# Performance work log

Hardware: AMD Instinct MI355X
Metric: run time of the kernel (lower is better)

## Reference

```python
import jax, jax.numpy as jnp
import numpy as np
from jax import lax

MIN_R = 0.01
RADIUS = 0.8
NSAMPLE = 32
PRED_NSAMPLE = 16
TEMPERATURE = 1.0
DIV_COEF = 10.0
GRID3 = 64  # grid_size**3, grid_size=4
EPS = 1e-5


def _ball_query(q, xyz, radius, nsample):
    """q (M,3), xyz (N,3), radius scalar or (M,). Returns idx (M,nsample) int32, empty (M,) bool.
    Mirrors stack ball_query CUDA op: first-found neighbors within radius, padded with first index."""
    N = xyz.shape[0]
    d2 = jnp.sum((q[:, None, :] - xyz[None, :, :]) ** 2, axis=-1)  # (M,N)
    r = jnp.broadcast_to(jnp.asarray(radius, d2.dtype), (q.shape[0],))[:, None]
    valid = d2 < r * r
    score = jnp.where(valid, -jnp.arange(N, dtype=jnp.int32), -(N + 1))
    vals, _ = lax.top_k(score, nsample)  # largest score == smallest valid index
    idx = -vals
    pad = idx == (N + 1)
    idx = jnp.where(pad, idx[:, :1], idx)  # pad with first found neighbor
    empty = pad[:, 0]                       # no neighbor at all
    idx = jnp.where(empty[:, None], 0, idx)
    return idx, empty


def _group(q, xyz, feats, idx, empty):
    """QueryAndGroup gather: relative xyz concat point features; zero empty queries.
    Returns (M, nsample, 3+C)."""
    g_xyz = xyz[idx] - q[:, None, :]
    g = jnp.concatenate([g_xyz, feats[idx]], axis=-1)
    return jnp.where(empty[:, None, None], jnp.zeros((), g.dtype), g)


def _mlp(x, params):
    """Shared 1x1 Conv2d + BatchNorm2d(training stats) + ReLU stack. x: (B,M,S,C)."""
    for W, g, b in params:
        x = jnp.einsum('bmsc,cd->bmsd', x, W)
        mu = x.mean(axis=(0, 1, 2))
        var = x.var(axis=(0, 1, 2))
        x = (x - mu) * lax.rsqrt(var + EPS) * g + b
        x = jax.nn.relu(x)
    return x


def setup_inputs() -> dict:
    key = jax.random.key(0)
    ks = jax.random.split(key, 16)
    B, N, C, R, Croi = 2, 8192, 32, 64, 128
    scene = jnp.array([10.0, 10.0, 4.0], jnp.float32)
    xyz = jax.random.uniform(ks[0], (B, N, 3), jnp.float32) * scene
    features = jax.random.normal(ks[1], (B, N, C), jnp.float32)
    rois = jax.random.uniform(ks[2], (B, R, GRID3, 3), jnp.float32) * scene
    roi_features = jax.random.normal(ks[3], (B, R, Croi), jnp.float32)

    def kaiming(k, fi, fo):
        return jax.random.normal(k, (fi, fo), jnp.float32) * np.float32(np.sqrt(2.0 / fi))

    return {
        'xyz': xyz, 'features': features, 'rois': rois, 'roi_features': roi_features,
        'temperature_decay': jnp.ones((1,), jnp.float32),
        # predict mlp: [32+3, 32, 32]
        'pw0': kaiming(ks[4], 35, 32), 'pg0': jnp.ones(32), 'pb0': jnp.zeros(32),
        'pw1': kaiming(ks[5], 32, 32), 'pg1': jnp.ones(32), 'pb1': jnp.zeros(32),
        # feat mlp: [32+3, 64, 64]
        'fw0': kaiming(ks[6], 35, 64), 'fg0': jnp.ones(64), 'fb0': jnp.zeros(64),
        'fw1': kaiming(ks[7], 64, 64), 'fg1': jnp.ones(64), 'fb1': jnp.zeros(64),
        # predict fc: [32*64 + 128, 1]
        'fcw': kaiming(ks[8], 2176, 1), 'fcb': jnp.zeros(1),
    }


def reference(xyz, features, rois, roi_features, temperature_decay,
              pw0, pg0, pb0, pw1, pg1, pb1,
              fw0, fg0, fb0, fw1, fg1, fb1, fcw, fcb):
    B, num_rois = rois.shape[0], rois.shape[1]
    new_xyz = rois.reshape(B, -1, 3)  # (B, M, 3), M = num_rois*grid^3

    # ---- radius-prediction branch: fixed-radius grouping + MLP + max-pool ----
    idx_p, empty_p = jax.vmap(lambda q, x: _ball_query(q, x, RADIUS, PRED_NSAMPLE))(new_xyz, xyz)
    gp = jax.vmap(_group)(new_xyz, xyz, features, idx_p, empty_p)  # (B,M,S,3+C)
    gp = _mlp(gp, [(pw0, pg0, pb0), (pw1, pg1, pb1)])
    pooled = gp.max(axis=2)                       # (B, M, Cp)
    pooled = pooled.reshape(B, num_rois, -1)      # (B, R, grid^3*Cp)
    res = jnp.concatenate([pooled, roi_features], axis=-1) @ fcw + fcb  # (B,R,1)
    r = jnp.maximum(res / DIV_COEF + RADIUS, MIN_R)
    r_pts = jnp.broadcast_to(r, (B, num_rois, GRID3)).reshape(B, -1)    # (B, M)

    # ---- deformable branch: per-query radius grouping + soft weights ----
    idx_d, empty_d = jax.vmap(lambda q, x, rr: _ball_query(q, x, rr, NSAMPLE))(new_xyz, xyz, r_pts)
    gd = jax.vmap(_group)(new_xyz, xyz, features, idx_d, empty_d)       # (B,M,S,3+C)
    dist = jnp.linalg.norm(gd[..., :3], axis=-1)                        # (B,M,S)
    w = jax.nn.sigmoid((r_pts[..., None] - dist) / (TEMPERATURE * temperature_decay[0]))
    w = jnp.where(empty_d[..., None], jnp.zeros((), w.dtype), w)
    gd = _mlp(gd, [(fw0, fg0, fb0), (fw1, fg1, fb1)])                   # (B,M,S,Cout)
    new_feats = (w[..., None] * gd).max(axis=2)                          # (B,M,Cout)

    return new_xyz.reshape(-1, 3), new_feats.reshape(-1, new_feats.shape[-1])
```

## Files before the change

### kernel.cpp

```cpp
#include <hip/hip_runtime.h>
#include <hip/hip_fp16.h>

#define NB 2
#define NPTS 8192
#define NQ 4096
#define MTOT 8192
#define SP 16
#define SD 32
#define CIN 32
#define CP 32
#define CF 64
#define NROI 128
#define RADIUS_C 0.8f
#define MIN_R_C 0.01f
#define DIV_COEF_C 10.0f

#define INV_CS 1.25f
#define NCX 13
#define NCY 13
#define NCZ 5
#define NCELL (NCX * NCY * NCZ)

__device__ int    g_idx_p[MTOT * SP];
__device__ int    g_empty_p[MTOT];
__device__ int    g_idx_d[MTOT * SD];
__device__ int    g_empty_d[MTOT];
__device__ int    g_cellcnt[NB][NCELL];
__device__ int    g_cellcur[NB][NCELL];
__device__ int    g_cellstart[NB][NCELL + 1];
__device__ float4 g_cellxyzw[NB][NPTS];
__device__ unsigned char g_xa[(size_t)MTOT * SD * CF * 2];
__device__ unsigned char g_xb[(size_t)MTOT * SD * CF * 2];
__device__ unsigned int g_w1h[CF * CF / 2];
__device__ float  g_psT[CF * 2048];
__device__ float  g_pqT[CF * 2048];
__device__ float  g_bnscale[4][CF];
__device__ float  g_bnshift[4][CF];
__device__ float  g_rroi[NROI];

typedef _Float16 h2v __attribute__((ext_vector_type(2)));
__device__ __forceinline__ float fdot2f(unsigned int a, unsigned int b, float c) {
#if defined(__has_builtin)
#if __has_builtin(__builtin_amdgcn_fdot2)
    h2v ha, hb;
    ha = *(h2v*)&a; hb = *(h2v*)&b;
    return __builtin_amdgcn_fdot2(ha, hb, c, false);
#else
    __half2 ha = *(__half2*)&a, hb = *(__half2*)&b;
    float2 fa = __half22float2(ha), fb = __half22float2(hb);
    return fmaf(fa.x, fb.x, fmaf(fa.y, fb.y, c));
#endif
#else
    __half2 ha = *(__half2*)&a, hb = *(__half2*)&b;
    float2 fa = __half22float2(ha), fb = __half22float2(hb);
    return fmaf(fa.x, fb.x, fmaf(fa.y, fb.y, c));
#endif
}

__device__ __forceinline__ int cell_of(float x, float y, float z) {
    int cx = min(NCX - 1, max(0, (int)floorf(x * INV_CS)));
    int cy = min(NCY - 1, max(0, (int)floorf(y * INV_CS)));
    int cz = min(NCZ - 1, max(0, (int)floorf(z * INV_CS)));
    return (cz * NCY + cy) * NCX + cx;
}

#define SETUP_N (MTOT * 3 + CF * CF / 2 + NB * NCELL)
__global__ void setup_kernel(const float* __restrict__ rois, const float* __restrict__ fw1,
                             float* __restrict__ out) {
    int i = blockIdx.x * 256 + threadIdx.x;
    if (i < MTOT * 3) { out[i] = rois[i]; return; }
    i -= MTOT * 3;
    if (i < CF * CF / 2) {
        int ch = i >> 5, c2 = i & 31;
        __half2 h = __floats2half2_rn(fw1[(2 * c2) * CF + ch], fw1[(2 * c2 + 1) * CF + ch]);
        g_w1h[i] = *(unsigned int*)&h;
        return;
    }
    i -= CF * CF / 2;
    if (i < NB * NCELL) ((int*)g_cellcnt)[i] = 0;
}

__global__ void grid_count_kernel(const float* __restrict__ xyz) {
    int i = blockIdx.x * 256 + threadIdx.x;
    int b = i >> 13;
    int cell = cell_of(xyz[(size_t)i * 3 + 0], xyz[(size_t)i * 3 + 1], xyz[(size_t)i * 3 + 2]);
    atomicAdd(&g_cellcnt[b][cell], 1);
}

__global__ void grid_prefix_kernel() {
    __shared__ int sc[1024];
    int b = blockIdx.x, tid = threadIdx.x;
    int v = (tid < NCELL) ? g_cellcnt[b][tid] : 0;
    sc[tid] = v;
    __syncthreads();
    for (int off = 1; off < 1024; off <<= 1) {
        int add = (tid >= off) ? sc[tid - off] : 0;
        __syncthreads();
        sc[tid] += add;
        __syncthreads();
    }
    if (tid < NCELL) {
        int excl = sc[tid] - v;
        g_cellstart[b][tid] = excl;
        g_cellcur[b][tid] = excl;
    }
    if (tid == 0) g_cellstart[b][NCELL] = NPTS;
}

__global__ void grid_scatter_kernel(const float* __restrict__ xyz) {
    int i = blockIdx.x * 256 + threadIdx.x;
    int b = i >> 13, il = i & (NPTS - 1);
    float x = xyz[(size_t)i * 3 + 0];
    float y = xyz[(size_t)i * 3 + 1];
    float z = xyz[(size_t)i * 3 + 2];
    int cell = cell_of(x, y, z);
    int pos = atomicAdd(&g_cellcur[b][cell], 1);
    g_cellxyzw[b][pos] = make_float4(x, y, z, __int_as_float(il));
}

template <int NS>
__launch_bounds__(256, 8)
__global__ void bq_grid_kernel(const float* __restrict__ xyz, const float* __restrict__ newxyz) {
    __shared__ int s_cand[4][512];
    __shared__ int s_meta[4][2];
    int tid = threadIdx.x, wv = tid >> 6, lane = tid & 63;
    int q = blockIdx.x * 4 + wv;
    int b = q >> 12;
    float qx = newxyz[q * 3 + 0], qy = newxyz[q * 3 + 1], qz = newxyz[q * 3 + 2];
    float r = (NS == SP) ? RADIUS_C : g_rroi[q >> 6];
    float r2 = r * r;
    int* idx_out   = (NS == SP) ? g_idx_p   : g_idx_d;
    int* empty_out = (NS == SP) ? g_empty_p : g_empty_d;

    if (lane == 0) s_meta[wv][0] = 0;
    __asm__ volatile("s_waitcnt lgkmcnt(0)" ::: "memory");

    float rp = r + 1e-4f;
    int xlo = max(0, min(NCX - 1, (int)floorf((qx - rp) * INV_CS)));
    int xhi = max(0, min(NCX - 1, (int)floorf((qx + rp) * INV_CS)));
    int ylo = max(0, min(NCY - 1, (int)floorf((qy - rp) * INV_CS)));
    int yhi = max(0, min(NCY - 1, (int)floorf((qy + rp) * INV_CS)));
    int zlo = max(0, min(NCZ - 1, (int)floorf((qz - rp) * INV_CS)));
    int zhi = max(0, min(NCZ - 1, (int)floorf((qz + rp) * INV_CS)));
    int nx = xhi - xlo + 1, ny = yhi - ylo + 1, nz = zhi - zlo + 1;
    int ncell = nx * ny * nz;

    bool ovf = false;
    for (int ci = lane; ci < ncell; ci += 64) {
        int cx = xlo + (ci % nx);
        int t1 = ci / nx;
        int cy = ylo + (t1 % ny);
        int cz = zlo + (t1 / ny);
        int cell = (cz * NCY + cy) * NCX + cx;
        int s0 = g_cellstart[b][cell], e0 = g_cellstart[b][cell + 1];
        for (int e = s0; e < e0; ++e) {
            float4 v = g_cellxyzw[b][e];
            float dx = qx - v.x, dy = qy - v.y, dz = qz - v.z;
            if (dx * dx + dy * dy + dz * dz < r2) {
                int pos = atomicAdd(&s_meta[wv][0], 1);
                if (pos < 512) s_cand[wv][pos] = __float_as_int(v.w);
                else ovf = true;
            }
        }
    }
    __asm__ volatile("s_waitcnt lgkmcnt(0) vmcnt(0)" ::: "memory");
    int cnt = s_meta[wv][0];

    if (__ballot(ovf)) {
        const float* xb = xyz + (size_t)b * NPTS * 3;
        int cnt2 = 0, first_idx = 0;
        for (int g = 0; g < NPTS / 64 && cnt2 < NS; ++g) {
            int p = (g << 6) + lane;
            float dx = qx - xb[3 * p + 0];
            float dy = qy - xb[3 * p + 1];
            float dz = qz - xb[3 * p + 2];
            bool valid = (dx * dx + dy * dy + dz * dz) < r2;
            unsigned long long mask = __ballot(valid);
            if (cnt2 == 0 && mask) first_idx = (g << 6) + (int)__builtin_ctzll(mask);
            int pos = cnt2 + __popcll(mask & ((1ull << lane) - 1ull));
            if (valid && pos < NS) idx_out[q * NS + pos] = p;
            cnt2 += (int)__popcll(mask);
        }
        if (cnt2 == 0) {
            if (lane < NS) idx_out[q * NS + lane] = 0;
            if (lane == 0) empty_out[q] = 1;
        } else {
            int filled = cnt2 < NS ? cnt2 : NS;
            if (lane >= filled && lane < NS) idx_out[q * NS + lane] = first_idx;
            if (lane == 0) empty_out[q] = 0;
        }
        return;
    }

    if (cnt == 0) {
        if (lane < NS) idx_out[q * NS + lane] = 0;
        if (lane == 0) empty_out[q] = 1;
        return;
    }
    for (int i = lane; i < cnt; i += 64) {
        int c = s_cand[wv][i];
        int rank = 0;
        for (int j = 0; j < cnt; ++j) rank += (s_cand[wv][j] < c) ? 1 : 0;
        if (rank < NS) idx_out[q * NS + rank] = c;
        if (rank == 0) s_meta[wv][1] = c;
    }
    __asm__ volatile("s_waitcnt lgkmcnt(0)" ::: "memory");
    if (cnt < NS && lane >= cnt && lane < NS) idx_out[q * NS + lane] = s_meta[wv][1];
    if (lane == 0) empty_out[q] = 0;
}

template <int NS, int CH, bool HALF>
__launch_bounds__(128, 4)
__global__ void mlp_passA_kernel(const float* __restrict__ xyz, const float* __restrict__ feats,
                                 const float* __restrict__ newxyz, const float* __restrict__ W0,
                                 void* __restrict__ xout_) {
    constexpr int GSTR = 37;
    constexpr int SST  = CH + 2;
    __shared__ float buf[128 * GSTR];
    __shared__ float ls[128], lq[128];
    int tid = threadIdx.x;
    int rowbase = blockIdx.x * 128;
    int row = rowbase + tid;
    int q = row / NS, b = q >> 12;
    const int* idx_arr = (NS == SP) ? g_idx_p : g_idx_d;
    const int* emp_arr = (NS == SP) ? g_empty_p : g_empty_d;
    {
        float* dst = &buf[tid * GSTR];
        if (emp_arr[q]) {
#pragma unroll
            for (int c = 0; c < 35; ++c) dst[c] = 0.f;
        } else {
            int idx = idx_arr[row];
            const float* xp = xyz + (size_t)b * NPTS * 3 + idx * 3;
            dst[0] = xp[0] - newxyz[q * 3 + 0];
            dst[1] = xp[1] - newxyz[q * 3 + 1];
            dst[2] = xp[2] - newxyz[q * 3 + 2];
            const float4* fp = (const float4*)(feats + (size_t)b * NPTS * CIN + (size_t)idx * CIN);
#pragma unroll
            for (int j = 0; j < 8; ++j) {
                float4 v = fp[j];
                dst[3 + 4 * j + 0] = v.x; dst[3 + 4 * j + 1] = v.y;
                dst[3 + 4 * j + 2] = v.z; dst[3 + 4 * j + 3] = v.w;
            }
        }
    }
    float acc[CH];
#pragma unroll
    for (int ch = 0; ch < CH; ++ch) acc[ch] = 0.f;
    {
        const float* inrow = &buf[tid * GSTR];
        for (int c = 0; c < 35; ++c) {
            float h = inrow[c];
#pragma unroll
            for (int ch = 0; ch < CH; ++ch) acc[ch] = fmaf(h, W0[c * CH + ch], acc[ch]);
        }
    }
    float* xf = (float*)xout_;
    __half* xh = (__half*)xout_;
    float sum = 0.f, sq = 0.f;
#pragma unroll
    for (int p = 0; p < 2; ++p) {
        __syncthreads();
        if ((tid >> 6) == p) {
            float* srow = &buf[(tid & 63) * SST];
#pragma unroll
            for (int ch = 0; ch < CH; ++ch) srow[ch] = acc[ch];
        }
        __syncthreads();
        if (CH == 64) {
            int ch = tid & 63, rg = tid >> 6;
            for (int r = 0; r < 32; ++r) {
                float v = buf[(rg * 32 + r) * SST + ch];
                size_t o = (size_t)(rowbase + p * 64 + rg * 32 + r) * CH + ch;
                if (HALF) xh[o] = __float2half_rn(v); else xf[o] = v;
                sum += v; sq += v * v;
            }
        } else {
            int ch = tid & 31, rg = tid >> 5;
            for (int r = 0; r < 16; ++r) {
                float v = buf[(rg * 16 + r) * SST + ch];
                size_t o = (size_t)(rowbase + p * 64 + rg * 16 + r) * CH + ch;
                if (HALF) xh[o] = __float2half_rn(v); else xf[o] = v;
                sum += v; sq += v * v;
            }
        }
    }
    ls[tid] = sum; lq[tid] = sq;
    __syncthreads();
    if (CH == 64) {
        if (tid < 64) {
            g_psT[tid * 2048 + blockIdx.x] = ls[tid] + ls[64 + tid];
            g_pqT[tid * 2048 + blockIdx.x] = lq[tid] + lq[64 + tid];
        }
    } else {
        if (tid < 32) {
            g_psT[tid * 2048 + blockIdx.x] = ls[tid] + ls[32 + tid] + ls[64 + tid] + ls[96 + tid];
            g_pqT[tid * 2048 + blockIdx.x] = lq[tid] + lq[32 + tid] + lq[64 + tid] + lq[96 + tid];
        }
    }
}

template <int NS, int CH>
__launch_bounds__(128, 4)
__global__ void mlp_passB_kernel(const float* __restrict__ W1, const float* __restrict__ xin,
                                 float* __restrict__ xout, int bn0) {
    constexpr int HSTR = 33;
    constexpr int SST  = CH + 2;
    __shared__ float buf[128 * 37];
    __shared__ float ls[128], lq[128];
    int tid = threadIdx.x;
    int rowbase = blockIdx.x * 128;
    const float* sc0 = g_bnscale[bn0];
    const float* sh0 = g_bnshift[bn0];
    float acc2[CH];
#pragma unroll
    for (int ch = 0; ch < CH; ++ch) acc2[ch] = 0.f;
    const float4* src = (const float4*)xin;
#pragma unroll
    for (int hc = 0; hc < CH / 32; ++hc) {
        if (hc) __syncthreads();
#pragma unroll
        for (int k = 0; k < 8; ++k) {
            int o4 = tid + k * 128;
            int rloc = o4 >> 3, j = o4 & 7;
            int c = 4 * j, gc = hc * 32 + c;
            float4 v = src[(size_t)(rowbase + rloc) * (CH / 4) + hc * 8 + j];
            float* d = &buf[rloc * HSTR + c];
            d[0] = fmaxf(fmaf(v.x, sc0[gc + 0], sh0[gc + 0]), 0.f);
            d[1] = fmaxf(fmaf(v.y, sc0[gc + 1], sh0[gc + 1]), 0.f);
            d[2] = fmaxf(fmaf(v.z, sc0[gc + 2], sh0[gc + 2]), 0.f);
            d[3] = fmaxf(fmaf(v.w, sc0[gc + 3], sh0[gc + 3]), 0.f);
        }
        __syncthreads();
        const float* hrow = &buf[tid * HSTR];
        for (int c = 0; c < 32; ++c) {
            float h = hrow[c];
#pragma unroll
            for (int ch = 0; ch < CH; ++ch)
                acc2[ch] = fmaf(h, W1[(hc * 32 + c) * CH + ch], acc2[ch]);
        }
    }
    float sum = 0.f, sq = 0.f;
#pragma unroll
    for (int p = 0; p < 2; ++p) {
        __syncthreads();
        if ((tid >> 6) == p) {
            float* srow = &buf[(tid & 63) * SST];
#pragma unroll
            for (int ch = 0; ch < CH; ++ch) srow[ch] = acc2[ch];
        }
        __syncthreads();
        int ch = tid & 31, rg = tid >> 5;
        for (int r = 0; r < 16; ++r) {
            float v = buf[(rg * 16 + r) * SST + ch];
            xout[(size_t)(rowbase + p * 64 + rg * 16 + r) * CH + ch] = v;
            sum += v; sq += v * v;
        }
    }
    ls[tid] = sum; lq[tid] = sq;
    __syncthreads();
    if (tid < 32) {
        g_psT[tid * 2048 + blockIdx.x] = ls[tid] + ls[32 + tid] + ls[64 + tid] + ls[96 + tid];
        g_pqT[tid * 2048 + blockIdx.x] = lq[tid] + lq[32 + tid] + lq[64 + tid] + lq[96 + tid];
    }
}

__launch_bounds__(128, 4)
__global__ void mlp_fB_kernel(const __half* __restrict__ xin, __half* __restrict__ xout) {
    __shared__ unsigned int hp[128 * 37];
    __shared__ float ls[128], lq[128];
    int tid = threadIdx.x;
    int rowbase = blockIdx.x * 128;
    const float* sc0 = g_bnscale[2];
    const float* sh0 = g_bnshift[2];
    {
        const float4* src = (const float4*)xin;
#pragma unroll
        for (int k = 0; k < 8; ++k) {
            int o4 = tid + k * 128;
            int rloc = o4 >> 3, j = o4 & 7;
            float4 v = src[(size_t)(rowbase + rloc) * 8 + j];
            const __half2* ph = (const __half2*)&v;
            unsigned int* d = &hp[rloc * 37 + 4 * j];
#pragma unroll
            for (int m = 0; m < 4; ++m) {
                float2 f = __half22float2(ph[m]);
                int gc = 8 * j + 2 * m;
                float a = fmaxf(fmaf(f.x, sc0[gc + 0], sh0[gc + 0]), 0.f);
                float bb = fmaxf(fmaf(f.y, sc0[gc + 1], sh0[gc + 1]), 0.f);
                __half2 hh = __floats2half2_rn(a, bb);
                d[m] = *(unsigned int*)&hh;
            }
        }
    }
    __syncthreads();
    float acc2[CF];
#pragma unroll
    for (int ch = 0; ch < CF; ++ch) acc2[ch] = 0.f;
    {
        const unsigned int* hrow = &hp[tid * 37];
#pragma unroll
        for (int c2 = 0; c2 < 32; ++c2) {
            unsigned int h2 = hrow[c2];
#pragma unroll
            for (int ch = 0; ch < CF; ++ch)
                acc2[ch] = fdot2f(h2, g_w1h[ch * 32 + c2], acc2[ch]);
        }
    }
    float* fview = (float*)hp;
    float sum = 0.f, sq = 0.f;
#pragma unroll
    for (int p = 0; p < 2; ++p) {
        __syncthreads();
        if ((tid >> 6) == p) {
            float* srow = &fview[(tid & 63) * 66];
#pragma unroll
            for (int ch = 0; ch < CF; ++ch) srow[ch] = acc2[ch];
        }
        __syncthreads();
        int ch = tid & 63, rg = tid >> 6;
        for (int r = 0; r < 32; ++r) {
            float v = fview[(rg * 32 + r) * 66 + ch];
            xout[(size_t)(rowbase + p * 64 + rg * 32 + r) * CF + ch] = __float2half_rn(v);
            sum += v; sq += v * v;
        }
    }
    ls[tid] = sum; lq[tid] = sq;
    __syncthreads();
    if (tid < 64) {
        g_psT[tid * 2048 + blockIdx.x] = ls[tid] + ls[64 + tid];
        g_pqT[tid * 2048 + blockIdx.x] = lq[tid] + lq[64 + tid];
    }
}

__global__ void finalize_kernel(const float* __restrict__ gamma, const float* __restrict__ beta,
                                float n, int layer, int nblocks) {
    __shared__ double l_s[256], l_q[256];
    int ch = blockIdx.x, tid = threadIdx.x;
    double s = 0, q = 0;
    for (int i = tid; i < nblocks; i += 256) { s += g_psT[ch * 2048 + i]; q += g_pqT[ch * 2048 + i]; }
    l_s[tid] = s; l_q[tid] = q; __syncthreads();
    for (int off = 128; off > 0; off >>= 1) {
        if (tid < off) { l_s[tid] += l_s[tid + off]; l_q[tid] += l_q[tid + off]; }
        __syncthreads();
    }
    if (tid == 0) {
        double mu = l_s[0] / (double)n;
        double var = l_q[0] / (double)n - mu * mu;
        if (var < 0) var = 0;
        double sc = (double)gamma[ch] / sqrt(var + 1e-5);
        g_bnscale[layer][ch] = (float)sc;
        g_bnshift[layer][ch] = (float)((double)beta[ch] - mu * sc);
    }
}

__global__ void passC_f_kernel(const float* __restrict__ xyz, const float* __restrict__ newxyz,
                               const float* __restrict__ td, const __half* __restrict__ xin,
                               float* __restrict__ out) {
    __shared__ float lw[64];
    int tid = threadIdx.x;
    int qpair = blockIdx.x * 2;
    if (tid < 64) {
        int ql = tid >> 5, s = tid & 31;
        int q = qpair + ql;
        float wv = 0.f;
        if (!g_empty_d[q]) {
            int idx = g_idx_d[q * SD + s];
            int b = q >> 12;
            float dx = xyz[(size_t)b * NPTS * 3 + idx * 3 + 0] - newxyz[q * 3 + 0];
            float dy = xyz[(size_t)b * NPTS * 3 + idx * 3 + 1] - newxyz[q * 3 + 1];
            float dz = xyz[(size_t)b * NPTS * 3 + idx * 3 + 2] - newxyz[q * 3 + 2];
            float dist = sqrtf(dx * dx + dy * dy + dz * dz);
            float rq = g_rroi[q >> 6];
            wv = 1.f / (1.f + expf(-(rq - dist) / td[0]));
        }
        lw[tid] = wv;
    }
    __syncthreads();
    int ql = tid >> 6, ch = tid & 63;
    int q = qpair + ql;
    float sc = g_bnscale[3][ch], sh = g_bnshift[3][ch];
    float m = 0.f;
    for (int s = 0; s < SD; ++s) {
        float v = __half2float(xin[((size_t)q * SD + s) * CF + ch]);
        m = fmaxf(m, lw[ql * 32 + s] * fmaxf(fmaf(v, sc, sh), 0.f));
    }
    out[MTOT * 3 + (size_t)q * CF + ch] = m;
}

__global__ void passC_roi_kernel(const float* __restrict__ fcw, const float* __restrict__ fcb,
                                 const float* __restrict__ roif, const float* __restrict__ xin) {
    __shared__ float red[256];
    int tid = threadIdx.x;
    int roi = blockIdx.x;
    int ch = tid & 31, qs = tid >> 5;
    float sc = g_bnscale[1][ch], sh = g_bnshift[1][ch];
    float acc = 0.f;
    for (int ql = qs; ql < 64; ql += 8) {
        int q = roi * 64 + ql;
        float m = 0.f;
        for (int s = 0; s < SP; ++s) {
            float v = xin[(size_t)(q * SP + s) * CP + ch] * sc + sh;
            m = fmaxf(m, fmaxf(v, 0.f));
        }
        acc += m * fcw[ql * CP + ch];
    }
    if (tid < 128) acc += roif[roi * 128 + tid] * fcw[2048 + tid];
    red[tid] = acc;
    __syncthreads();
    for (int off = 128; off > 0; off >>= 1) {
        if (tid < off) red[tid] += red[tid + off];
        __syncthreads();
    }
    if (tid == 0)
        g_rroi[roi] = fmaxf((red[0] + fcb[0]) / DIV_COEF_C + RADIUS_C, MIN_R_C);
}

extern "C" void kernel_launch(void* const* d_in, const int* in_sizes, int n_in,
                              void* d_out, int out_size, void* d_ws, size_t ws_size,
                              hipStream_t stream) {
    const float* xyz   = (const float*)d_in[0];
    const float* feats = (const float*)d_in[1];
    const float* rois  = (const float*)d_in[2];
    const float* roif  = (const float*)d_in[3];
    const float* td    = (const float*)d_in[4];
    const float* pw0 = (const float*)d_in[5];
    const float* pg0 = (const float*)d_in[6];
    const float* pb0 = (const float*)d_in[7];
    const float* pw1 = (const float*)d_in[8];
    const float* pg1 = (const float*)d_in[9];
    const float* pb1 = (const float*)d_in[10];
    const float* fw0 = (const float*)d_in[11];
    const float* fg0 = (const float*)d_in[12];
    const float* fb0 = (const float*)d_in[13];
    const float* fw1 = (const float*)d_in[14];
    const float* fg1 = (const float*)d_in[15];
    const float* fb1 = (const float*)d_in[16];
    const float* fcw = (const float*)d_in[17];
    const float* fcb = (const float*)d_in[18];
    float* out = (float*)d_out;

    void* xa; hipGetSymbolAddress(&xa, HIP_SYMBOL(g_xa));
    void* xb; hipGetSymbolAddress(&xb, HIP_SYMBOL(g_xb));

    setup_kernel<<<(SETUP_N + 255) / 256, 256, 0, stream>>>(rois, fw1, out);
    grid_count_kernel<<<64, 256, 0, stream>>>(xyz);
    grid_prefix_kernel<<<2, 1024, 0, stream>>>();
    grid_scatter_kernel<<<64, 256, 0, stream>>>(xyz);

    bq_grid_kernel<SP><<<MTOT / 4, 256, 0, stream>>>(xyz, rois);
    mlp_passA_kernel<SP, CP, false><<<1024, 128, 0, stream>>>(xyz, feats, rois, pw0, xa);
    finalize_kernel<<<CP, 256, 0, stream>>>(pg0, pb0, (float)(MTOT * SP), 0, 1024);
    mlp_passB_kernel<SP, CP><<<1024, 128, 0, stream>>>(pw1, (const float*)xa, (float*)xb, 0);
    finalize_kernel<<<CP, 256, 0, stream>>>(pg1, pb1, (float)(MTOT * SP), 1, 1024);
    passC_roi_kernel<<<NROI, 256, 0, stream>>>(fcw, fcb, roif, (const float*)xb);

    bq_grid_kernel<SD><<<MTOT / 4, 256, 0, stream>>>(xyz, rois);
    mlp_passA_kernel<SD, CF, true><<<2048, 128, 0, stream>>>(xyz, feats, rois, fw0, xa);
    finalize_kernel<<<CF, 256, 0, stream>>>(fg0, fb0, (float)(MTOT * SD), 2, 2048);
    mlp_fB_kernel<<<2048, 128, 0, stream>>>((const __half*)xa, (__half*)xb);
    finalize_kernel<<<CF, 256, 0, stream>>>(fg1, fb1, (float)(MTOT * SD), 3, 2048);
    passC_f_kernel<<<MTOT / 2, 128, 0, stream>>>(xyz, rois, td, (const __half*)xb, out);
}
```

Before: 272.1 us.

## Fuse grid ball query into first MLP pass kernel with shared-memory indices

Merges the grid-based ball-query kernel into the first MLP pass, so each 256-thread block computes neighbor indices for its queries into LDS and then gathers and applies the first layer directly. This removes two kernel launches and the global round trip of index/empty arrays for the pooling branch, while the deform branch still writes indices for later use. Blocks grow to 256 threads with more rows each, halving the partial-stat count for the BN finalize. The trade-off is serialized per-wave query loops inside the block and larger LDS use, which may lower occupancy.

```diff
diff --git a/kernel.cpp b/kernel.cpp
--- a/kernel.cpp
+++ b/kernel.cpp
@@ -21,8 +21,6 @@
 #define NCZ 5
 #define NCELL (NCX * NCY * NCZ)
 
-__device__ int    g_idx_p[MTOT * SP];
-__device__ int    g_empty_p[MTOT];
 __device__ int    g_idx_d[MTOT * SD];
 __device__ int    g_empty_d[MTOT];
 __device__ int    g_cellcnt[NB][NCELL];
@@ -118,124 +116,131 @@
     g_cellxyzw[b][pos] = make_float4(x, y, z, __int_as_float(il));
 }
 
-template <int NS>
-__launch_bounds__(256, 8)
-__global__ void bq_grid_kernel(const float* __restrict__ xyz, const float* __restrict__ newxyz) {
-    __shared__ int s_cand[4][512];
-    __shared__ int s_meta[4][2];
-    int tid = threadIdx.x, wv = tid >> 6, lane = tid & 63;
-    int q = blockIdx.x * 4 + wv;
-    int b = q >> 12;
-    float qx = newxyz[q * 3 + 0], qy = newxyz[q * 3 + 1], qz = newxyz[q * 3 + 2];
-    float r = (NS == SP) ? RADIUS_C : g_rroi[q >> 6];
-    float r2 = r * r;
-    int* idx_out   = (NS == SP) ? g_idx_p   : g_idx_d;
-    int* empty_out = (NS == SP) ? g_empty_p : g_empty_d;
-
-    if (lane == 0) s_meta[wv][0] = 0;
-    __asm__ volatile("s_waitcnt lgkmcnt(0)" ::: "memory");
-
-    float rp = r + 1e-4f;
-    int xlo = max(0, min(NCX - 1, (int)floorf((qx - rp) * INV_CS)));
-    int xhi = max(0, min(NCX - 1, (int)floorf((qx + rp) * INV_CS)));
-    int ylo = max(0, min(NCY - 1, (int)floorf((qy - rp) * INV_CS)));
-    int yhi = max(0, min(NCY - 1, (int)floorf((qy + rp) * INV_CS)));
-    int zlo = max(0, min(NCZ - 1, (int)floorf((qz - rp) * INV_CS)));
-    int zhi = max(0, min(NCZ - 1, (int)floorf((qz + rp) * INV_CS)));
-    int nx = xhi - xlo + 1, ny = yhi - ylo + 1, nz = zhi - zlo + 1;
-    int ncell = nx * ny * nz;
-
-    bool ovf = false;
-    for (int ci = lane; ci < ncell; ci += 64) {
-        int cx = xlo + (ci % nx);
-        int t1 = ci / nx;
-        int cy = ylo + (t1 % ny);
-        int cz = zlo + (t1 / ny);
-        int cell = (cz * NCY + cy) * NCX + cx;
-        int s0 = g_cellstart[b][cell], e0 = g_cellstart[b][cell + 1];
-        for (int e = s0; e < e0; ++e) {
-            float4 v = g_cellxyzw[b][e];
-            float dx = qx - v.x, dy = qy - v.y, dz = qz - v.z;
-            if (dx * dx + dy * dy + dz * dz < r2) {
-                int pos = atomicAdd(&s_meta[wv][0], 1);
-                if (pos < 512) s_cand[wv][pos] = __float_as_int(v.w);
-                else ovf = true;
-            }
-        }
-    }
-    __asm__ volatile("s_waitcnt lgkmcnt(0) vmcnt(0)" ::: "memory");
-    int cnt = s_meta[wv][0];
-
-    if (__ballot(ovf)) {
-        const float* xb = xyz + (size_t)b * NPTS * 3;
-        int cnt2 = 0, first_idx = 0;
-        for (int g = 0; g < NPTS / 64 && cnt2 < NS; ++g) {
-            int p = (g << 6) + lane;
-            float dx = qx - xb[3 * p + 0];
-            float dy = qy - xb[3 * p + 1];
-            float dz = qz - xb[3 * p + 2];
-            bool valid = (dx * dx + dy * dy + dz * dz) < r2;
-            unsigned long long mask = __ballot(valid);
-            if (cnt2 == 0 && mask) first_idx = (g << 6) + (int)__builtin_ctzll(mask);
-            int pos = cnt2 + __popcll(mask & ((1ull << lane) - 1ull));
-            if (valid && pos < NS) idx_out[q * NS + pos] = p;
-            cnt2 += (int)__popcll(mask);
-        }
-        if (cnt2 == 0) {
-            if (lane < NS) idx_out[q * NS + lane] = 0;
-            if (lane == 0) empty_out[q] = 1;
-        } else {
-            int filled = cnt2 < NS ? cnt2 : NS;
-            if (lane >= filled && lane < NS) idx_out[q * NS + lane] = first_idx;
-            if (lane == 0) empty_out[q] = 0;
-        }
-        return;
-    }
-
-    if (cnt == 0) {
-        if (lane < NS) idx_out[q * NS + lane] = 0;
-        if (lane == 0) empty_out[q] = 1;
-        return;
-    }
-    for (int i = lane; i < cnt; i += 64) {
-        int c = s_cand[wv][i];
-        int rank = 0;
-        for (int j = 0; j < cnt; ++j) rank += (s_cand[wv][j] < c) ? 1 : 0;
-        if (rank < NS) idx_out[q * NS + rank] = c;
-        if (rank == 0) s_meta[wv][1] = c;
-    }
-    __asm__ volatile("s_waitcnt lgkmcnt(0)" ::: "memory");
-    if (cnt < NS && lane >= cnt && lane < NS) idx_out[q * NS + lane] = s_meta[wv][1];
-    if (lane == 0) empty_out[q] = 0;
-}
-
 template <int NS, int CH, bool HALF>
-__launch_bounds__(128, 4)
-__global__ void mlp_passA_kernel(const float* __restrict__ xyz, const float* __restrict__ feats,
-                                 const float* __restrict__ newxyz, const float* __restrict__ W0,
-                                 void* __restrict__ xout_) {
+__launch_bounds__(256, 4)
+__global__ void fusedA_kernel(const float* __restrict__ xyz, const float* __restrict__ feats,
+                              const float* __restrict__ newxyz, const float* __restrict__ W0,
+                              void* __restrict__ xout_) {
+    constexpr int NQPB = 256 / NS;
+    constexpr int QPW  = NQPB / 4;
     constexpr int GSTR = 37;
     constexpr int SST  = CH + 2;
-    __shared__ float buf[128 * GSTR];
-    __shared__ float ls[128], lq[128];
-    int tid = threadIdx.x;
-    int rowbase = blockIdx.x * 128;
-    int row = rowbase + tid;
-    int q = row / NS, b = q >> 12;
-    const int* idx_arr = (NS == SP) ? g_idx_p : g_idx_d;
-    const int* emp_arr = (NS == SP) ? g_empty_p : g_empty_d;
+    __shared__ float buf[256 * GSTR];
+    int* s_cand  = (int*)buf;
+    int* l_idx   = (int*)((char*)buf + 8192);
+    int* l_empty = (int*)((char*)buf + 9216);
+    int* s_meta  = (int*)((char*)buf + 9280);
+    float* ls    = (float*)((char*)buf + 20480);
+    float* lq    = (float*)((char*)buf + 24576);
+
+    int tid = threadIdx.x, wv = tid >> 6, lane = tid & 63;
+    int qbase = blockIdx.x * NQPB;
+    int rowbase = blockIdx.x * 256;
+
+    for (int i = 0; i < QPW; ++i) {
+        int ql = wv * QPW + i;
+        int q = qbase + ql;
+        int b = q >> 12;
+        float qx = newxyz[q * 3 + 0], qy = newxyz[q * 3 + 1], qz = newxyz[q * 3 + 2];
+        float r = (NS == SP) ? RADIUS_C : g_rroi[q >> 6];
+        float r2 = r * r;
+        if (lane == 0) s_meta[wv * 2 + 0] = 0;
+        __asm__ volatile("s_waitcnt lgkmcnt(0)" ::: "memory");
+
+        float rp = r + 1e-4f;
+        int xlo = max(0, min(NCX - 1, (int)floorf((qx - rp) * INV_CS)));
+        int xhi = max(0, min(NCX - 1, (int)floorf((qx + rp) * INV_CS)));
+        int ylo = max(0, min(NCY - 1, (int)floorf((qy - rp) * INV_CS)));
+        int yhi = max(0, min(NCY - 1, (int)floorf((qy + rp) * INV_CS)));
+        int zlo = max(0, min(NCZ - 1, (int)floorf((qz - rp) * INV_CS)));
+        int zhi = max(0, min(NCZ - 1, (int)floorf((qz + rp) * INV_CS)));
+        int nx = xhi - xlo + 1, ny = yhi - ylo + 1, nz = zhi - zlo + 1;
+        int ncell = nx * ny * nz;
+
+        bool ovf = false;
+        for (int ci = lane; ci < ncell; ci += 64) {
+            int cx = xlo + (ci % nx);
+            int t1 = ci / nx;
+            int cy = ylo + (t1 % ny);
+            int cz = zlo + (t1 / ny);
+            int cell = (cz * NCY + cy) * NCX + cx;
+            int s0 = g_cellstart[b][cell], e0 = g_cellstart[b][cell + 1];
+            for (int e = s0; e < e0; ++e) {
+                float4 v = g_cellxyzw[b][e];
+                float dx = qx - v.x, dy = qy - v.y, dz = qz - v.z;
+                if (dx * dx + dy * dy + dz * dz < r2) {
+                    int pos = atomicAdd(&s_meta[wv * 2 + 0], 1);
+                    if (pos < 512) s_cand[wv * 512 + pos] = __float_as_int(v.w);
+                    else ovf = true;
+                }
+            }
+        }
+        __asm__ volatile("s_waitcnt lgkmcnt(0) vmcnt(0)" ::: "memory");
+        int cnt = s_meta[wv * 2 + 0];
+
+        if (__ballot(ovf)) {
+            const float* xb = xyz + (size_t)b * NPTS * 3;
+            int cnt2 = 0, first_idx = 0;
+            for (int g = 0; g < NPTS / 64 && cnt2 < NS; ++g) {
+                int p = (g << 6) + lane;
+                float dx = qx - xb[3 * p + 0];
+                float dy = qy - xb[3 * p + 1];
+                float dz = qz - xb[3 * p + 2];
+                bool valid = (dx * dx + dy * dy + dz * dz) < r2;
+                unsigned long long mask = __ballot(valid);
+                if (cnt2 == 0 && mask) first_idx = (g << 6) + (int)__builtin_ctzll(mask);
+                int pos = cnt2 + __popcll(mask & ((1ull << lane) - 1ull));
+                if (valid && pos < NS) l_idx[ql * NS + pos] = p;
+                cnt2 += (int)__popcll(mask);
+            }
+            if (cnt2 == 0) {
+                if (lane < NS) l_idx[ql * NS + lane] = 0;
+                if (lane == 0) l_empty[ql] = 1;
+            } else {
+                int filled = cnt2 < NS ? cnt2 : NS;
+                if (lane >= filled && lane < NS) l_idx[ql * NS + lane] = first_idx;
+                if (lane == 0) l_empty[ql] = 0;
+            }
+        } else if (cnt == 0) {
+            if (lane < NS) l_idx[ql * NS + lane] = 0;
+            if (lane == 0) l_empty[ql] = 1;
+        } else {
+            for (int ii = lane; ii < cnt; ii += 64) {
+                int c = s_cand[wv * 512 + ii];
+                int rank = 0;
+                for (int j = 0; j < cnt; ++j) rank += (s_cand[wv * 512 + j] < c) ? 1 : 0;
+                if (rank < NS) l_idx[ql * NS + rank] = c;
+                if (rank == 0) s_meta[wv * 2 + 1] = c;
+            }
+            __asm__ volatile("s_waitcnt lgkmcnt(0)" ::: "memory");
+            if (cnt < NS && lane >= cnt && lane < NS) l_idx[ql * NS + lane] = s_meta[wv * 2 + 1];
+            if (lane == 0) l_empty[ql] = 0;
+        }
+    }
+    __syncthreads();
+
+    if (NS == SD) {
+        g_idx_d[rowbase + tid] = l_idx[tid];
+        if (tid < NQPB) g_empty_d[qbase + tid] = l_empty[tid];
+    }
+    int myql = tid / NS;
+    int q = qbase + myql;
+    int b = q >> 12;
+    int myempty = l_empty[myql];
+    int myidx = l_idx[tid];
+    __syncthreads();
+
     {
         float* dst = &buf[tid * GSTR];
-        if (emp_arr[q]) {
+        if (myempty) {
 #pragma unroll
             for (int c = 0; c < 35; ++c) dst[c] = 0.f;
         } else {
-            int idx = idx_arr[row];
-            const float* xp = xyz + (size_t)b * NPTS * 3 + idx * 3;
+            const float* xp = xyz + (size_t)b * NPTS * 3 + myidx * 3;
             dst[0] = xp[0] - newxyz[q * 3 + 0];
             dst[1] = xp[1] - newxyz[q * 3 + 1];
             dst[2] = xp[2] - newxyz[q * 3 + 2];
-            const float4* fp = (const float4*)(feats + (size_t)b * NPTS * CIN + (size_t)idx * CIN);
+            const float4* fp = (const float4*)(feats + (size_t)b * NPTS * CIN + (size_t)myidx * CIN);
 #pragma unroll
             for (int j = 0; j < 8; ++j) {
                 float4 v = fp[j];
@@ -259,7 +264,7 @@
     __half* xh = (__half*)xout_;
     float sum = 0.f, sq = 0.f;
 #pragma unroll
-    for (int p = 0; p < 2; ++p) {
+    for (int p = 0; p < 4; ++p) {
         __syncthreads();
         if ((tid >> 6) == p) {
             float* srow = &buf[(tid & 63) * SST];
@@ -269,33 +274,36 @@
         __syncthreads();
         if (CH == 64) {
             int ch = tid & 63, rg = tid >> 6;
-            for (int r = 0; r < 32; ++r) {
-                float v = buf[(rg * 32 + r) * SST + ch];
-                size_t o = (size_t)(rowbase + p * 64 + rg * 32 + r) * CH + ch;
-                if (HALF) xh[o] = __float2half_rn(v); else xf[o] = v;
-                sum += v; sq += v * v;
-            }
-        } else {
-            int ch = tid & 31, rg = tid >> 5;
             for (int r = 0; r < 16; ++r) {
                 float v = buf[(rg * 16 + r) * SST + ch];
                 size_t o = (size_t)(rowbase + p * 64 + rg * 16 + r) * CH + ch;
                 if (HALF) xh[o] = __float2half_rn(v); else xf[o] = v;
                 sum += v; sq += v * v;
             }
+        } else {
+            int ch = tid & 31, rg = tid >> 5;
+            for (int r = 0; r < 8; ++r) {
+                float v = buf[(rg * 8 + r) * SST + ch];
+                size_t o = (size_t)(rowbase + p * 64 + rg * 8 + r) * CH + ch;
+                if (HALF) xh[o] = __float2half_rn(v); else xf[o] = v;
+                sum += v; sq += v * v;
+            }
         }
     }
     ls[tid] = sum; lq[tid] = sq;
     __syncthreads();
     if (CH == 64) {
         if (tid < 64) {
-            g_psT[tid * 2048 + blockIdx.x] = ls[tid] + ls[64 + tid];
-            g_pqT[tid * 2048 + blockIdx.x] = lq[tid] + lq[64 + tid];
+            g_psT[tid * 2048 + blockIdx.x] = ls[tid] + ls[64 + tid] + ls[128 + tid] + ls[192 + tid];
+            g_pqT[tid * 2048 + blockIdx.x] = lq[tid] + lq[64 + tid] + lq[128 + tid] + lq[192 + tid];
         }
     } else {
         if (tid < 32) {
-            g_psT[tid * 2048 + blockIdx.x] = ls[tid] + ls[32 + tid] + ls[64 + tid] + ls[96 + tid];
-            g_pqT[tid * 2048 + blockIdx.x] = lq[tid] + lq[32 + tid] + lq[64 + tid] + lq[96 + tid];
+            float s = 0.f, qq = 0.f;
+#pragma unroll
+            for (int k = 0; k < 8; ++k) { s += ls[tid + 32 * k]; qq += lq[tid + 32 * k]; }
+            g_psT[tid * 2048 + blockIdx.x] = s;
+            g_pqT[tid * 2048 + blockIdx.x] = qq;
         }
     }
 }
@@ -548,16 +556,14 @@
     grid_prefix_kernel<<<2, 1024, 0, stream>>>();
     grid_scatter_kernel<<<64, 256, 0, stream>>>(xyz);
 
-    bq_grid_kernel<SP><<<MTOT / 4, 256, 0, stream>>>(xyz, rois);
-    mlp_passA_kernel<SP, CP, false><<<1024, 128, 0, stream>>>(xyz, feats, rois, pw0, xa);
-    finalize_kernel<<<CP, 256, 0, stream>>>(pg0, pb0, (float)(MTOT * SP), 0, 1024);
+    fusedA_kernel<SP, CP, false><<<512, 256, 0, stream>>>(xyz, feats, rois, pw0, xa);
+    finalize_kernel<<<CP, 256, 0, stream>>>(pg0, pb0, (float)(MTOT * SP), 0, 512);
     mlp_passB_kernel<SP, CP><<<1024, 128, 0, stream>>>(pw1, (const float*)xa, (float*)xb, 0);
     finalize_kernel<<<CP, 256, 0, stream>>>(pg1, pb1, (float)(MTOT * SP), 1, 1024);
     passC_roi_kernel<<<NROI, 256, 0, stream>>>(fcw, fcb, roif, (const float*)xb);
 
-    bq_grid_kernel<SD><<<MTOT / 4, 256, 0, stream>>>(xyz, rois);
-    mlp_passA_kernel<SD, CF, true><<<2048, 128, 0, stream>>>(xyz, feats, rois, fw0, xa);
-    finalize_kernel<<<CF, 256, 0, stream>>>(fg0, fb0, (float)(MTOT * SD), 2, 2048);
+    fusedA_kernel<SD, CF, true><<<1024, 256, 0, stream>>>(xyz, feats, rois, fw0, xa);
+    finalize_kernel<<<CF, 256, 0, stream>>>(fg0, fb0, (float)(MTOT * SD), 2, 1024);
     mlp_fB_kernel<<<2048, 128, 0, stream>>>((const __half*)xa, (__half*)xb);
     finalize_kernel<<<CF, 256, 0, stream>>>(fg1, fb1, (float)(MTOT * SD), 3, 2048);
     passC_f_kernel<<<MTOT / 2, 128, 0, stream>>>(xyz, rois, td, (const __half*)xb, out);
```

Measured after the change: 281.0 us. 1.03x slower.

## Split output channels across two thread halves in MLP pass kernels

Applied to the files above, without the earlier changes.

The first-layer MLP kernels and the half-precision second-layer kernel now launch 256 threads per block instead of 128. Each group of 128 threads computes half of the output channels for the same 128 rows, and the gather is split across the halves too. This halves the per-thread accumulator arrays to cut register pressure and raise occupancy, and it doubles the threads available for the store and statistics loops. The cost is redundant shared-memory row reads across the two halves and a larger partial-sum reduction.

```diff
diff --git a/kernel.cpp b/kernel.cpp
--- a/kernel.cpp
+++ b/kernel.cpp
@@ -210,49 +210,55 @@
 }
 
 template <int NS, int CH, bool HALF>
-__launch_bounds__(128, 4)
+__launch_bounds__(256, 6)
 __global__ void mlp_passA_kernel(const float* __restrict__ xyz, const float* __restrict__ feats,
                                  const float* __restrict__ newxyz, const float* __restrict__ W0,
                                  void* __restrict__ xout_) {
     constexpr int GSTR = 37;
     constexpr int SST  = CH + 2;
+    constexpr int CHH  = CH / 2;
     __shared__ float buf[128 * GSTR];
-    __shared__ float ls[128], lq[128];
+    __shared__ float ls[256], lq[256];
     int tid = threadIdx.x;
+    int row = tid & 127, half = tid >> 7;
     int rowbase = blockIdx.x * 128;
-    int row = rowbase + tid;
-    int q = row / NS, b = q >> 12;
+    int grow = rowbase + row;
+    int q = grow / NS, b = q >> 12;
     const int* idx_arr = (NS == SP) ? g_idx_p : g_idx_d;
     const int* emp_arr = (NS == SP) ? g_empty_p : g_empty_d;
     {
-        float* dst = &buf[tid * GSTR];
+        float* dst = &buf[row * GSTR];
         if (emp_arr[q]) {
-#pragma unroll
-            for (int c = 0; c < 35; ++c) dst[c] = 0.f;
+            int c0 = half ? 18 : 0, c1 = half ? 35 : 18;
+            for (int c = c0; c < c1; ++c) dst[c] = 0.f;
         } else {
-            int idx = idx_arr[row];
-            const float* xp = xyz + (size_t)b * NPTS * 3 + idx * 3;
-            dst[0] = xp[0] - newxyz[q * 3 + 0];
-            dst[1] = xp[1] - newxyz[q * 3 + 1];
-            dst[2] = xp[2] - newxyz[q * 3 + 2];
+            int idx = idx_arr[grow];
+            if (half == 0) {
+                const float* xp = xyz + (size_t)b * NPTS * 3 + idx * 3;
+                dst[0] = xp[0] - newxyz[q * 3 + 0];
+                dst[1] = xp[1] - newxyz[q * 3 + 1];
+                dst[2] = xp[2] - newxyz[q * 3 + 2];
+            }
             const float4* fp = (const float4*)(feats + (size_t)b * NPTS * CIN + (size_t)idx * CIN);
 #pragma unroll
-            for (int j = 0; j < 8; ++j) {
-                float4 v = fp[j];
-                dst[3 + 4 * j + 0] = v.x; dst[3 + 4 * j + 1] = v.y;
-                dst[3 + 4 * j + 2] = v.z; dst[3 + 4 * j + 3] = v.w;
+            for (int j = 0; j < 4; ++j) {
+                float4 v = fp[half * 4 + j];
+                float* d = dst + 3 + (half * 4 + j) * 4;
+                d[0] = v.x; d[1] = v.y; d[2] = v.z; d[3] = v.w;
             }
         }
     }
-    float acc[CH];
-#pragma unroll
-    for (int ch = 0; ch < CH; ++ch) acc[ch] = 0.f;
+    __syncthreads();
+    float acc[CHH];
+#pragma unroll
+    for (int ch = 0; ch < CHH; ++ch) acc[ch] = 0.f;
     {
-        const float* inrow = &buf[tid * GSTR];
+        const float* inrow = &buf[row * GSTR];
+        const float* w = W0 + half * CHH;
         for (int c = 0; c < 35; ++c) {
             float h = inrow[c];
 #pragma unroll
-            for (int ch = 0; ch < CH; ++ch) acc[ch] = fmaf(h, W0[c * CH + ch], acc[ch]);
+            for (int ch = 0; ch < CHH; ++ch) acc[ch] = fmaf(h, w[c * CH + ch], acc[ch]);
         }
     }
     float* xf = (float*)xout_;
@@ -261,41 +267,44 @@
 #pragma unroll
     for (int p = 0; p < 2; ++p) {
         __syncthreads();
-        if ((tid >> 6) == p) {
-            float* srow = &buf[(tid & 63) * SST];
-#pragma unroll
-            for (int ch = 0; ch < CH; ++ch) srow[ch] = acc[ch];
+        if ((row >> 6) == p) {
+            float* srow = &buf[(row & 63) * SST + half * CHH];
+#pragma unroll
+            for (int ch = 0; ch < CHH; ++ch) srow[ch] = acc[ch];
         }
         __syncthreads();
         if (CH == 64) {
             int ch = tid & 63, rg = tid >> 6;
-            for (int r = 0; r < 32; ++r) {
-                float v = buf[(rg * 32 + r) * SST + ch];
-                size_t o = (size_t)(rowbase + p * 64 + rg * 32 + r) * CH + ch;
-                if (HALF) xh[o] = __float2half_rn(v); else xf[o] = v;
-                sum += v; sq += v * v;
-            }
-        } else {
-            int ch = tid & 31, rg = tid >> 5;
             for (int r = 0; r < 16; ++r) {
                 float v = buf[(rg * 16 + r) * SST + ch];
                 size_t o = (size_t)(rowbase + p * 64 + rg * 16 + r) * CH + ch;
                 if (HALF) xh[o] = __float2half_rn(v); else xf[o] = v;
                 sum += v; sq += v * v;
             }
+        } else {
+            int ch = tid & 31, rg = tid >> 5;
+            for (int r = 0; r < 8; ++r) {
+                float v = buf[(rg * 8 + r) * SST + ch];
+                size_t o = (size_t)(rowbase + p * 64 + rg * 8 + r) * CH + ch;
+                if (HALF) xh[o] = __float2half_rn(v); else xf[o] = v;
+                sum += v; sq += v * v;
+            }
         }
     }
     ls[tid] = sum; lq[tid] = sq;
     __syncthreads();
     if (CH == 64) {
         if (tid < 64) {
-            g_psT[tid * 2048 + blockIdx.x] = ls[tid] + ls[64 + tid];
-            g_pqT[tid * 2048 + blockIdx.x] = lq[tid] + lq[64 + tid];
+            g_psT[tid * 2048 + blockIdx.x] = ls[tid] + ls[64 + tid] + ls[128 + tid] + ls[192 + tid];
+            g_pqT[tid * 2048 + blockIdx.x] = lq[tid] + lq[64 + tid] + lq[128 + tid] + lq[192 + tid];
         }
     } else {
         if (tid < 32) {
-            g_psT[tid * 2048 + blockIdx.x] = ls[tid] + ls[32 + tid] + ls[64 + tid] + ls[96 + tid];
-            g_pqT[tid * 2048 + blockIdx.x] = lq[tid] + lq[32 + tid] + lq[64 + tid] + lq[96 + tid];
+            float s = 0.f, qq = 0.f;
+#pragma unroll
+            for (int k = 0; k < 8; ++k) { s += ls[tid + 32 * k]; qq += lq[tid + 32 * k]; }
+            g_psT[tid * 2048 + blockIdx.x] = s;
+            g_pqT[tid * 2048 + blockIdx.x] = qq;
         }
     }
 }
@@ -365,23 +374,24 @@
     }
 }
 
-__launch_bounds__(128, 4)
+__launch_bounds__(256, 6)
 __global__ void mlp_fB_kernel(const __half* __restrict__ xin, __half* __restrict__ xout) {
-    __shared__ unsigned int hp[128 * 37];
-    __shared__ float ls[128], lq[128];
+    __shared__ unsigned int hp[128 * 33];
+    __shared__ float ls[256], lq[256];
     int tid = threadIdx.x;
+    int row = tid & 127, half = tid >> 7;
     int rowbase = blockIdx.x * 128;
     const float* sc0 = g_bnscale[2];
     const float* sh0 = g_bnshift[2];
     {
         const float4* src = (const float4*)xin;
 #pragma unroll
-        for (int k = 0; k < 8; ++k) {
-            int o4 = tid + k * 128;
+        for (int k = 0; k < 4; ++k) {
+            int o4 = tid + k * 256;
             int rloc = o4 >> 3, j = o4 & 7;
             float4 v = src[(size_t)(rowbase + rloc) * 8 + j];
             const __half2* ph = (const __half2*)&v;
-            unsigned int* d = &hp[rloc * 37 + 4 * j];
+            unsigned int* d = &hp[rloc * 33 + 4 * j];
 #pragma unroll
             for (int m = 0; m < 4; ++m) {
                 float2 f = __half22float2(ph[m]);
@@ -394,17 +404,18 @@
         }
     }
     __syncthreads();
-    float acc2[CF];
-#pragma unroll
-    for (int ch = 0; ch < CF; ++ch) acc2[ch] = 0.f;
+    float acc[32];
+#pragma unroll
+    for (int ch = 0; ch < 32; ++ch) acc[ch] = 0.f;
     {
-        const unsigned int* hrow = &hp[tid * 37];
+        const unsigned int* hrow = &hp[row * 33];
+        const unsigned int* wbase = g_w1h + (half * 32) * 32;
 #pragma unroll
         for (int c2 = 0; c2 < 32; ++c2) {
             unsigned int h2 = hrow[c2];
 #pragma unroll
-            for (int ch = 0; ch < CF; ++ch)
-                acc2[ch] = fdot2f(h2, g_w1h[ch * 32 + c2], acc2[ch]);
+            for (int ch = 0; ch < 32; ++ch)
+                acc[ch] = fdot2f(h2, wbase[ch * 32 + c2], acc[ch]);
         }
     }
     float* fview = (float*)hp;
@@ -412,24 +423,24 @@
 #pragma unroll
     for (int p = 0; p < 2; ++p) {
         __syncthreads();
-        if ((tid >> 6) == p) {
-            float* srow = &fview[(tid & 63) * 66];
-#pragma unroll
-            for (int ch = 0; ch < CF; ++ch) srow[ch] = acc2[ch];
+        if ((row >> 6) == p) {
+            float* srow = &fview[(row & 63) * 66 + half * 32];
+#pragma unroll
+            for (int ch = 0; ch < 32; ++ch) srow[ch] = acc[ch];
         }
         __syncthreads();
         int ch = tid & 63, rg = tid >> 6;
-        for (int r = 0; r < 32; ++r) {
-            float v = fview[(rg * 32 + r) * 66 + ch];
-            xout[(size_t)(rowbase + p * 64 + rg * 32 + r) * CF + ch] = __float2half_rn(v);
+        for (int r = 0; r < 16; ++r) {
+            float v = fview[(rg * 16 + r) * 66 + ch];
+            xout[(size_t)(rowbase + p * 64 + rg * 16 + r) * CF + ch] = __float2half_rn(v);
             sum += v; sq += v * v;
         }
     }
     ls[tid] = sum; lq[tid] = sq;
     __syncthreads();
     if (tid < 64) {
-        g_psT[tid * 2048 + blockIdx.x] = ls[tid] + ls[64 + tid];
-        g_pqT[tid * 2048 + blockIdx.x] = lq[tid] + lq[64 + tid];
+        g_psT[tid * 2048 + blockIdx.x] = ls[tid] + ls[64 + tid] + ls[128 + tid] + ls[192 + tid];
+        g_pqT[tid * 2048 + blockIdx.x] = lq[tid] + lq[64 + tid] + lq[128 + tid] + lq[192 + tid];
     }
 }
 
@@ -549,16 +560,16 @@
     grid_scatter_kernel<<<64, 256, 0, stream>>>(xyz);
 
     bq_grid_kernel<SP><<<MTOT / 4, 256, 0, stream>>>(xyz, rois);
-    mlp_passA_kernel<SP, CP, false><<<1024, 128, 0, stream>>>(xyz, feats, rois, pw0, xa);
+    mlp_passA_kernel<SP, CP, false><<<1024, 256, 0, stream>>>(xyz, feats, rois, pw0, xa);
     finalize_kernel<<<CP, 256, 0, stream>>>(pg0, pb0, (float)(MTOT * SP), 0, 1024);
     mlp_passB_kernel<SP, CP><<<1024, 128, 0, stream>>>(pw1, (const float*)xa, (float*)xb, 0);
     finalize_kernel<<<CP, 256, 0, stream>>>(pg1, pb1, (float)(MTOT * SP), 1, 1024);
     passC_roi_kernel<<<NROI, 256, 0, stream>>>(fcw, fcb, roif, (const float*)xb);
 
     bq_grid_kernel<SD><<<MTOT / 4, 256, 0, stream>>>(xyz, rois);
-    mlp_passA_kernel<SD, CF, true><<<2048, 128, 0, stream>>>(xyz, feats, rois, fw0, xa);
+    mlp_passA_kernel<SD, CF, true><<<2048, 256, 0, stream>>>(xyz, feats, rois, fw0, xa);
     finalize_kernel<<<CF, 256, 0, stream>>>(fg0, fb0, (float)(MTOT * SD), 2, 2048);
-    mlp_fB_kernel<<<2048, 128, 0, stream>>>((const __half*)xa, (__half*)xb);
+    mlp_fB_kernel<<<2048, 256, 0, stream>>>((const __half*)xa, (__half*)xb);
     finalize_kernel<<<CF, 256, 0, stream>>>(fg1, fb1, (float)(MTOT * SD), 3, 2048);
     passC_f_kernel<<<MTOT / 2, 128, 0, stream>>>(xyz, rois, td, (const __half*)xb, out);
 }
```

After: 380.0 us. 39.7% more time.
